# Performance work log

Measured on AMD Instinct MI355X. Metric: run time of the kernel, lower is better.

## Reference

```python
import jax, jax.numpy as jnp
import numpy as np

# ---- static geometry derived from truncation (matches torch __init__) ----
T = 127
N_LAT_NH = T + 1                                   # 128 NH latitudes
LONS = [20 + 4 * i for i in range(N_LAT_NH)]       # octahedral reduced grid
CUMS = np.concatenate([[0], np.cumsum(np.array(LONS + LONS[::-1]))]).astype(int)
HZW_NH = np.minimum(4 + np.arange(N_LAT_NH), T)    # cubic truncation: m_max = nlon//4 - 1, capped at T
N_LATS_PER_M = np.array([(HZW_NH >= m).sum() for m in range(T + 1)])
L_SYM_FULL = (T + 3) // 2                          # 65 rows before dropping row 0
L_ANT = (T + 2) // 2                               # 64
N_VARS = 128
BATCH, ENS = 4, 1


def _tri_masks():
    """Zero-padded triangular structure of the per-m Legendre matrices."""
    sym = np.zeros((T + 1, L_SYM_FULL, N_LAT_NH), np.float32)
    ant = np.zeros((T + 1, L_ANT, N_LAT_NH), np.float32)
    for m in range(T + 1):
        n_lats = int(N_LATS_PER_M[m])
        ms = (T - m + 3) // 2
        off = L_SYM_FULL - ms
        sym[m, off:, N_LAT_NH - n_lats:] = 1.0
        if (m + 1) % 2 == 1:
            sym[m, off, :] = 0.0
        ma = (T - m + 2) // 2
        off = L_ANT - ma
        ant[m, off:, N_LAT_NH - n_lats:] = 1.0
        if m % 2 == 1:
            ant[m, off, :] = 0.0
    return sym[:, 1:, :], ant   # module drops first symmetric row -> [128,64,128]


def setup_inputs() -> dict:
    key = jax.random.key(0)
    k1, k2, k3 = jax.random.split(key, 3)
    n_grid = int(CUMS[-1])
    x = jax.random.normal(k1, (BATCH, ENS, n_grid, N_VARS), jnp.float32)
    sm, am = _tri_masks()
    # random stand-ins for (gaussian-weight-fused) Legendre polynomials, with the exact
    # triangular zero structure the module builds from ecTrans assets
    symmetric = jax.random.normal(k2, sm.shape, jnp.float32) * jnp.asarray(sm)
    antisymmetric = jax.random.normal(k3, am.shape, jnp.float32) * jnp.asarray(am)
    return {"x": x, "symmetric": symmetric, "antisymmetric": antisymmetric}


def reference(x, symmetric, antisymmetric):
    """Octahedral SHT forward: ragged longitudinal rfft -> hemispheric fold -> per-m Legendre matmuls.

    Returns spectrum [b, e, l, m, vars, 2] (real/imag stacked on last axis).
    """
    n_lat = 2 * N_LAT_NH
    north, south = [], []
    # loop is over structurally distinct (ragged) latitude ring lengths; NH lat i and its
    # SH mirror (lat n_lat-1-i) share nlon/truncation, so batch them in one FFT call.
    for i in range(N_LAT_NH):
        j = n_lat - 1 - i
        nlon = LONS[i]
        xn = x[:, :, CUMS[i]:CUMS[i + 1], :]           # [b,e,nlon,v]
        xs = x[:, :, CUMS[j]:CUMS[j + 1], :]
        xp = jnp.stack([xn, xs], axis=2)               # [b,e,2,nlon,v]
        f = jnp.fft.rfft(xp, axis=3) / nlon            # torch norm='forward'
        m_hi = int(HZW_NH[i]) + 1                      # keep m <= highest zonal wavenumber
        f = f[:, :, :, :m_hi, :]
        f = jnp.pad(f, ((0, 0), (0, 0), (0, 0), (0, T + 1 - m_hi), (0, 0)))
        north.append(f[:, :, 0])
        south.append(f[:, :, 1])                       # index i <-> lat n_lat-1-i: already pole-mirrored
    north = jnp.stack(north, axis=2)                   # [b,e,n_lat_nh,m,v] complex64
    south = jnp.stack(south, axis=2)
    # hemispheric symmetry of Legendre polynomials
    sym = north + south
    anti = north - south
    # per-m truncated Legendre contractions over NH latitudes (n)
    out_s = jnp.einsum('mln,benmv->belmv', symmetric, sym)     # [b,e,64,m,v]
    out_a = jnp.einsum('mln,benmv->belmv', antisymmetric, anti)
    # interleave symmetric (l-m even) and antisymmetric (l-m odd) rows -> full l axis (128)
    spec = jnp.stack([out_s, out_a], axis=3)
    b, e, L, _, M, V = spec.shape
    spec = spec.reshape(b, e, 2 * L, M, V)             # [b,e,l,m,v] complex, lower triangle zeros
    return jnp.stack([spec.real, spec.imag], axis=-1)  # real view [b,e,l,m,v,2]
```

## Files before the change

### kernel.cpp

```cpp
#include <hip/hip_runtime.h>
#include <hip/hip_bf16.h>

#define NGRID 70144
#define NV 128

typedef float f32x4 __attribute__((ext_vector_type(4)));
typedef short short8 __attribute__((ext_vector_type(8)));

__device__ __forceinline__ float4 f4add(float4 a, float4 b){ return make_float4(a.x+b.x, a.y+b.y, a.z+b.z, a.w+b.w); }
__device__ __forceinline__ float4 f4sub(float4 a, float4 b){ return make_float4(a.x-b.x, a.y-b.y, a.z-b.z, a.w-b.w); }

__device__ __forceinline__ unsigned f2bf(float f){
  return (unsigned)__bfloat16_as_ushort(__float2bfloat16(f));
}
__device__ __forceinline__ float bf2f(unsigned h){ return __uint_as_float(h<<16); }
__device__ __forceinline__ unsigned packsplit(float f){
  unsigned h = f2bf(f);
  unsigned l = f2bf(f - bf2f(h));
  return (h<<16) | l;
}
__device__ __forceinline__ int swzc(int c){ return (c ^ (c>>3)) & 7; }

__device__ __forceinline__ void unpack_frag(int4 a, int4 b, short8 &bh, short8 &bl){
  int h0 = (int)(((unsigned)a.x >> 16) | ((unsigned)a.y & 0xFFFF0000u));
  int h1 = (int)(((unsigned)a.z >> 16) | ((unsigned)a.w & 0xFFFF0000u));
  int h2 = (int)(((unsigned)b.x >> 16) | ((unsigned)b.y & 0xFFFF0000u));
  int h3 = (int)(((unsigned)b.z >> 16) | ((unsigned)b.w & 0xFFFF0000u));
  int l0 = (int)(((unsigned)a.x & 0xFFFFu) | ((unsigned)a.y << 16));
  int l1 = (int)(((unsigned)a.z & 0xFFFFu) | ((unsigned)a.w << 16));
  int l2 = (int)(((unsigned)b.x & 0xFFFFu) | ((unsigned)b.y << 16));
  int l3 = (int)(((unsigned)b.z & 0xFFFFu) | ((unsigned)b.w << 16));
  int4 H = make_int4(h0,h1,h2,h3), L = make_int4(l0,l1,l2,l3);
  bh = *(short8*)&H; bl = *(short8*)&L;
}

struct TileT { unsigned char ring, type, mc; };
constexpr int calc_ntiles(){
  int n=0;
  for(int r=0;r<128;r++){
    int mhi=(5+r<128)?(5+r):128;
    int mtn=(mhi+15)/16;
    n += 2*((mtn+3)/4);
  }
  return n;
}
constexpr int NTILES = calc_ntiles();
struct Tiles { TileT t[NTILES]; };
constexpr Tiles make_tiles(){
  Tiles T{}; int k=0;
  for(int r=127;r>=0;r--){
    int mhi=(5+r<128)?(5+r):128;
    int mtn=(mhi+15)/16;
    int nc=(mtn+3)/4;
    for(int mc=0;mc<nc;mc++)
      for(int tp=0;tp<2;tp++){
        T.t[k].ring=(unsigned char)r; T.t[k].type=(unsigned char)tp; T.t[k].mc=(unsigned char)mc; k++;
      }
  }
  return T;
}
__constant__ Tiles TILES = make_tiles();

struct Offs { long o[129]; };
constexpr Offs make_offs(){
  Offs O{}; long off=0;
  for(int r=0;r<128;r++){
    O.o[r]=off;
    int mh=(5+r<128)?(5+r):128, jc=11+2*r;
    off += 4L*(((mh+15)/16)*16)*(((jc+31)/32)*32);
  }
  O.o[128]=off;
  return O;
}
__constant__ Offs TWOFF = make_offs();
constexpr long TWATOT = make_offs().o[128];

__global__ void fill_tw(unsigned short* __restrict__ twA){
  int ring = blockIdx.x, t = blockIdx.y;
  int N = 20+4*ring, H = N/2, JC = H+1;
  int mhi = (5+ring<128)?(5+ring):128;
  int Mpad = ((mhi+15)>>4)<<4;
  int Kpad = ((JC+31)>>5)<<5;
  long MK = (long)Mpad*Kpad;
  unsigned short* hiT = twA + TWOFF.o[ring] + (long)(t*2)*MK;
  unsigned short* loT = hiT + MK;
  float invN = 1.0f/(float)N;
  int tid = threadIdx.x;
  for(int m=0;m<Mpad;m++){
    int p0   = (int)(((long)m*tid) % N);
    int step = (int)(((long)m*256) % N);
    int p = p0;
    for(int j=tid;j<Kpad;j+=256){
      float val = 0.f;
      if(m < mhi && j < JC){
        float th = 6.2831853071795864f * (float)p * invN;
        float sn, cs; __sincosf(th,&sn,&cs);
        val = (t ? -sn : cs) * invN;
      }
      unsigned h = f2bf(val);
      unsigned l = f2bf(val - bf2f(h));
      long idx = (long)m*Kpad + j;
      hiT[idx] = (unsigned short)h;
      loT[idx] = (unsigned short)l;
      p += step; if(p>=N) p-=N;
    }
  }
}

__global__ __launch_bounds__(256,3) void dft_mfma(const float* __restrict__ x,
                                                  const unsigned short* __restrict__ twA,
                                                  unsigned* __restrict__ Gp){
  TileT tl = TILES.t[blockIdx.x];
  int ring = tl.ring, type = tl.type;
  int b = blockIdx.y;
  int N = 20+4*ring, H = N/2, JC = H+1;
  int mhi = (5+ring<128)?(5+ring):128;
  int MtN = (mhi+15)>>4;
  int Mt0 = tl.mc*4;
  int KT = (JC+31)>>5;
  int Kpad = KT<<5;
  int Mpad = MtN<<4;

  long MK = (long)Mpad*Kpad;
  const unsigned short* Ahi = twA + TWOFF.o[ring] + (long)(type*2)*MK;
  const unsigned short* Alo = Ahi + MK;

  const float* xn = x + ((long)b*NGRID + (long)ring*(2*ring+18))*NV;
  long a1 = ring+1;
  const float* xs = x + ((long)b*NGRID + (NGRID - a1*(2*a1+18)))*NV;

  __shared__ __align__(16) unsigned Bp[8192];

  int tid = threadIdx.x;
  int jb = tid >> 5, vp = tid & 31;
  int wave = tid >> 6, lane = tid & 63;
  int jj = lane & 15, kb = lane >> 4;

  f32x4 acc[4][4];
  #pragma unroll
  for(int Mt=0;Mt<4;Mt++)
    #pragma unroll
    for(int ct=0;ct<4;ct++) acc[Mt][ct] = (f32x4){0.f,0.f,0.f,0.f};

  for(int kt=0; kt<KT; ++kt){
    __syncthreads();
    float4 fS[4], fA[4];
    #pragma unroll
    for(int dj=0;dj<4;dj++){
      int j = kt*32 + jb*4 + dj;
      float4 z = make_float4(0.f,0.f,0.f,0.f);
      float4 nj=z, sj=z, np=z, sp=z;
      if(j < JC){
        nj = *(const float4*)&xn[(long)j*NV + vp*4];
        sj = *(const float4*)&xs[(long)j*NV + vp*4];
        if(j > 0 && j < H){
          int jp = N - j;
          np = *(const float4*)&xn[(long)jp*NV + vp*4];
          sp = *(const float4*)&xs[(long)jp*NV + vp*4];
        }
      }
      float4 e  = f4add(nj, sj), o  = f4sub(nj, sj);
      float4 ep = f4add(np, sp), op = f4sub(np, sp);
      fS[dj] = type ? f4sub(e, ep) : f4add(e, ep);
      fA[dj] = type ? f4sub(o, op) : f4add(o, op);
    }
    #pragma unroll
    for(int dv=0;dv<4;dv++){
      int c0 = (vp*4+dv)*2;
      int4 wS = make_int4((int)packsplit(((const float*)&fS[0])[dv]),
                          (int)packsplit(((const float*)&fS[1])[dv]),
                          (int)packsplit(((const float*)&fS[2])[dv]),
                          (int)packsplit(((const float*)&fS[3])[dv]));
      *(int4*)&Bp[c0*32 + ((jb*4) ^ (swzc(c0)<<2))] = wS;
      int c1 = c0 + 1;
      int4 wA = make_int4((int)packsplit(((const float*)&fA[0])[dv]),
                          (int)packsplit(((const float*)&fA[1])[dv]),
                          (int)packsplit(((const float*)&fA[2])[dv]),
                          (int)packsplit(((const float*)&fA[3])[dv]));
      *(int4*)&Bp[c1*32 + ((jb*4) ^ (swzc(c1)<<2))] = wA;
    }
    __syncthreads();
    short8 bh[4], bl[4];
    #pragma unroll
    for(int ct=0;ct<4;ct++){
      int c = wave*64 + ct*16 + jj;
      int sw = swzc(c)<<2;
      int4 pa = *(const int4*)&Bp[c*32 + ((kb*8) ^ sw)];
      int4 pb = *(const int4*)&Bp[c*32 + ((kb*8+4) ^ sw)];
      unpack_frag(pa, pb, bh[ct], bl[ct]);
    }
    #pragma unroll
    for(int Mt=0;Mt<4;Mt++){
      if(Mt0+Mt < MtN){
        long ao = (long)((Mt0+Mt)*16 + jj)*Kpad + kt*32 + kb*8;
        short8 ah = *(const short8*)&Ahi[ao];
        short8 al = *(const short8*)&Alo[ao];
        #pragma unroll
        for(int ct=0;ct<4;ct++){
          acc[Mt][ct] = __builtin_amdgcn_mfma_f32_16x16x32_bf16(ah, bh[ct], acc[Mt][ct], 0,0,0);
          acc[Mt][ct] = __builtin_amdgcn_mfma_f32_16x16x32_bf16(al, bh[ct], acc[Mt][ct], 0,0,0);
          acc[Mt][ct] = __builtin_amdgcn_mfma_f32_16x16x32_bf16(ah, bl[ct], acc[Mt][ct], 0,0,0);
        }
      }
    }
  }
  #pragma unroll
  for(int Mt=0;Mt<4;Mt++){
    if(Mt0+Mt < MtN){
      #pragma unroll
      for(int ct=0;ct<4;ct++){
        int c = wave*64 + ct*16 + jj;
        int s = c & 1, v = c >> 1;
        #pragma unroll
        for(int reg=0;reg<4;reg++){
          int m = (Mt0+Mt)*16 + (kb<<2) + reg;
          if(m < mhi){
            Gp[(long)((s*2+type)*128 + m)*65536 + (long)ring*512 + b*128 + v]
              = packsplit(acc[Mt][ct][reg]);
          }
        }
      }
    }
  }
}

__global__ void w_split(const float* __restrict__ Wsym, const float* __restrict__ Want,
                        unsigned short* __restrict__ Wh, unsigned short* __restrict__ Wl){
  long i = (long)blockIdx.x*256 + threadIdx.x;
  const float* W = (i < 1048576) ? Wsym : Want;
  float w = W[i & 1048575];
  unsigned h = f2bf(w);
  unsigned l = f2bf(w - bf2f(h));
  Wh[i] = (unsigned short)h;
  Wl[i] = (unsigned short)l;
}

__global__ __launch_bounds__(256) void legendre_mfma(const unsigned short* __restrict__ Wh,
                                                     const unsigned short* __restrict__ Wl,
                                                     const unsigned* __restrict__ Gp,
                                                     float* __restrict__ out){
  int m = blockIdx.x, b = blockIdx.y, s = blockIdx.z;
  __shared__ __align__(16) unsigned Bp[8192];
  int tid = threadIdx.x;
  int wave = tid >> 6, lane = tid & 63;
  int jj = lane & 15, kb = lane >> 4;

  int kt0 = (m > 4) ? ((m-4) >> 5) : 0;

  const unsigned short* WA = Wh + (long)(s*128+m)*8192;
  const unsigned short* WB = Wl + (long)(s*128+m)*8192;
  int ri = tid & 1, v = tid >> 1;
  long gC0 = (long)((s*2+ri)*128 + m)*65536 + (long)b*128 + v;

  f32x4 acc[4][4];
  #pragma unroll
  for(int a=0;a<4;a++)
    #pragma unroll
    for(int q=0;q<4;q++) acc[a][q] = (f32x4){0.f,0.f,0.f,0.f};

  int swT = swzc(tid)<<2;
  for(int kt=kt0; kt<4; ++kt){
    __syncthreads();
    #pragma unroll
    for(int k4=0;k4<32;k4+=4){
      int4 w = make_int4((int)Gp[gC0 + (long)(kt*32+k4+0)*512],
                         (int)Gp[gC0 + (long)(kt*32+k4+1)*512],
                         (int)Gp[gC0 + (long)(kt*32+k4+2)*512],
                         (int)Gp[gC0 + (long)(kt*32+k4+3)*512]);
      *(int4*)&Bp[tid*32 + (k4 ^ swT)] = w;
    }
    __syncthreads();
    short8 bh[4], bl[4];
    #pragma unroll
    for(int nt=0;nt<4;nt++){
      int c = (wave*4+nt)*16 + jj;
      int sw = swzc(c)<<2;
      int4 pa = *(const int4*)&Bp[c*32 + ((kb*8) ^ sw)];
      int4 pb = *(const int4*)&Bp[c*32 + ((kb*8+4) ^ sw)];
      unpack_frag(pa, pb, bh[nt], bl[nt]);
    }
    #pragma unroll
    for(int Mt=0;Mt<4;Mt++){
      long ao = (long)(Mt*16 + jj)*128 + kt*32 + kb*8;
      short8 ah = *(const short8*)&WA[ao];
      short8 al = *(const short8*)&WB[ao];
      #pragma unroll
      for(int nt=0;nt<4;nt++){
        acc[Mt][nt] = __builtin_amdgcn_mfma_f32_16x16x32_bf16(ah, bh[nt], acc[Mt][nt], 0,0,0);
        acc[Mt][nt] = __builtin_amdgcn_mfma_f32_16x16x32_bf16(al, bh[nt], acc[Mt][nt], 0,0,0);
        acc[Mt][nt] = __builtin_amdgcn_mfma_f32_16x16x32_bf16(ah, bl[nt], acc[Mt][nt], 0,0,0);
      }
    }
  }
  int r4 = (lane>>4)<<2;
  #pragma unroll
  for(int Mt=0;Mt<4;Mt++){
    #pragma unroll
    for(int nt=0;nt<4;nt++){
      int c = (wave*4+nt)*16 + jj;
      #pragma unroll
      for(int reg=0;reg<4;reg++){
        int l = Mt*16 + r4 + reg;
        out[((long)(b*128 + 2*l + s)*128 + m)*256 + c] = acc[Mt][nt][reg];
      }
    }
  }
}

extern "C" void kernel_launch(void* const* d_in, const int* in_sizes, int n_in,
                              void* d_out, int out_size, void* d_ws, size_t ws_size,
                              hipStream_t stream) {
  const float* x    = (const float*)d_in[0];
  const float* Wsym = (const float*)d_in[1];
  const float* Want = (const float*)d_in[2];
  float* out = (float*)d_out;

  size_t gpOffB = (size_t)TWATOT*2;
  if(gpOffB < 8388608) gpOffB = 8388608;
  gpOffB = (gpOffB + 255) & ~(size_t)255;

  unsigned short* twA = (unsigned short*)d_ws;
  unsigned* Gp = (unsigned*)((char*)d_ws + gpOffB);
  unsigned short* Wh = (unsigned short*)d_ws;
  unsigned short* Wl = Wh + 2097152;

  hipLaunchKernelGGL(fill_tw,       dim3(128,2),     dim3(256), 0, stream, twA);
  hipLaunchKernelGGL(dft_mfma,      dim3(NTILES,4),  dim3(256), 0, stream, x, twA, Gp);
  hipLaunchKernelGGL(w_split,       dim3(8192),      dim3(256), 0, stream, Wsym, Want, Wh, Wl);
  hipLaunchKernelGGL(legendre_mfma, dim3(128,4,2),   dim3(256), 0, stream, Wh, Wl, Gp, out);
}
```

Baseline: 386.5 us.

## Split DFT tiles by variable half, group rings, parallelize twiddle fill

Each DFT tile now covers half of the 128 variables, which halves the accumulators and the LDS staging buffer and doubles the number of blocks. Tiles are grouped in sets of 8 rings with padding slots that exit early, interleaving variants across neighbouring rings. The twiddle-fill kernel is also split across 4 m-slices to add parallelism. The aim is higher occupancy and better load balance. The cost is that the twiddle matrix A is loaded twice and there are more global loads of float2 width.

```diff
diff --git a/kernel.cpp b/kernel.cpp
--- a/kernel.cpp
+++ b/kernel.cpp
@@ -6,9 +6,6 @@
 
 typedef float f32x4 __attribute__((ext_vector_type(4)));
 typedef short short8 __attribute__((ext_vector_type(8)));
-
-__device__ __forceinline__ float4 f4add(float4 a, float4 b){ return make_float4(a.x+b.x, a.y+b.y, a.z+b.z, a.w+b.w); }
-__device__ __forceinline__ float4 f4sub(float4 a, float4 b){ return make_float4(a.x-b.x, a.y-b.y, a.z-b.z, a.w-b.w); }
 
 __device__ __forceinline__ unsigned f2bf(float f){
   return (unsigned)__bfloat16_as_ushort(__float2bfloat16(f));
@@ -34,27 +31,41 @@
   bh = *(short8*)&H; bl = *(short8*)&L;
 }
 
-struct TileT { unsigned char ring, type, mc; };
+struct TileT { unsigned char ring, mc, type, vh; };
+constexpr int nvar_of(int r){
+  int mhi=(5+r<128)?(5+r):128;
+  int mtn=(mhi+15)/16;
+  int nch=(mtn+3)/4;
+  return nch*4;
+}
 constexpr int calc_ntiles(){
-  int n=0;
-  for(int r=0;r<128;r++){
-    int mhi=(5+r<128)?(5+r):128;
-    int mtn=(mhi+15)/16;
-    n += 2*((mtn+3)/4);
-  }
-  return n;
+  int tot=0;
+  for(int g=0; g<16; g++){
+    int mv=0;
+    for(int q=0;q<8;q++){ int nv=nvar_of(127-(g*8+q)); if(nv>mv) mv=nv; }
+    tot += 8*mv;
+  }
+  return tot;
 }
 constexpr int NTILES = calc_ntiles();
 struct Tiles { TileT t[NTILES]; };
 constexpr Tiles make_tiles(){
   Tiles T{}; int k=0;
-  for(int r=127;r>=0;r--){
-    int mhi=(5+r<128)?(5+r):128;
-    int mtn=(mhi+15)/16;
-    int nc=(mtn+3)/4;
-    for(int mc=0;mc<nc;mc++)
-      for(int tp=0;tp<2;tp++){
-        T.t[k].ring=(unsigned char)r; T.t[k].type=(unsigned char)tp; T.t[k].mc=(unsigned char)mc; k++;
+  for(int g=0; g<16; g++){
+    int mv=0;
+    for(int q=0;q<8;q++){ int nv=nvar_of(127-(g*8+q)); if(nv>mv) mv=nv; }
+    for(int var=0; var<mv; var++)
+      for(int q=0;q<8;q++){
+        int r = 127-(g*8+q);
+        if(var < nvar_of(r)){
+          T.t[k].ring=(unsigned char)r;
+          T.t[k].mc  =(unsigned char)(var>>2);
+          T.t[k].type=(unsigned char)((var>>1)&1);
+          T.t[k].vh  =(unsigned char)(var&1);
+        } else {
+          T.t[k].ring=255;
+        }
+        k++;
       }
   }
   return T;
@@ -76,7 +87,7 @@
 constexpr long TWATOT = make_offs().o[128];
 
 __global__ void fill_tw(unsigned short* __restrict__ twA){
-  int ring = blockIdx.x, t = blockIdx.y;
+  int ring = blockIdx.x, t = blockIdx.y, mq = blockIdx.z;
   int N = 20+4*ring, H = N/2, JC = H+1;
   int mhi = (5+ring<128)?(5+ring):128;
   int Mpad = ((mhi+15)>>4)<<4;
@@ -86,7 +97,7 @@
   unsigned short* loT = hiT + MK;
   float invN = 1.0f/(float)N;
   int tid = threadIdx.x;
-  for(int m=0;m<Mpad;m++){
+  for(int m=mq; m<Mpad; m+=4){
     int p0   = (int)(((long)m*tid) % N);
     int step = (int)(((long)m*256) % N);
     int p = p0;
@@ -107,11 +118,12 @@
   }
 }
 
-__global__ __launch_bounds__(256,3) void dft_mfma(const float* __restrict__ x,
-                                                  const unsigned short* __restrict__ twA,
-                                                  unsigned* __restrict__ Gp){
+__global__ __launch_bounds__(256) void dft_mfma(const float* __restrict__ x,
+                                                const unsigned short* __restrict__ twA,
+                                                unsigned* __restrict__ Gp){
   TileT tl = TILES.t[blockIdx.x];
-  int ring = tl.ring, type = tl.type;
+  if(tl.ring == 255) return;
+  int ring = tl.ring, type = tl.type, vh = tl.vh;
   int b = blockIdx.y;
   int N = 20+4*ring, H = N/2, JC = H+1;
   int mhi = (5+ring<128)?(5+ring):128;
@@ -129,61 +141,65 @@
   long a1 = ring+1;
   const float* xs = x + ((long)b*NGRID + (NGRID - a1*(2*a1+18)))*NV;
 
-  __shared__ __align__(16) unsigned Bp[8192];
+  __shared__ __align__(16) unsigned Bp[4096];
 
   int tid = threadIdx.x;
-  int jb = tid >> 5, vp = tid & 31;
+  int jb = tid >> 5;
+  int vp = tid & 31;
+  int vo = vh*64 + vp*2;
   int wave = tid >> 6, lane = tid & 63;
   int jj = lane & 15, kb = lane >> 4;
 
-  f32x4 acc[4][4];
+  f32x4 acc[4][2];
   #pragma unroll
-  for(int Mt=0;Mt<4;Mt++)
-    #pragma unroll
-    for(int ct=0;ct<4;ct++) acc[Mt][ct] = (f32x4){0.f,0.f,0.f,0.f};
+  for(int Mt=0;Mt<4;Mt++){ acc[Mt][0]=(f32x4){0.f,0.f,0.f,0.f}; acc[Mt][1]=(f32x4){0.f,0.f,0.f,0.f}; }
 
   for(int kt=0; kt<KT; ++kt){
     __syncthreads();
-    float4 fS[4], fA[4];
+    float gSx[4], gSy[4], gAx[4], gAy[4];
     #pragma unroll
     for(int dj=0;dj<4;dj++){
       int j = kt*32 + jb*4 + dj;
-      float4 z = make_float4(0.f,0.f,0.f,0.f);
-      float4 nj=z, sj=z, np=z, sp=z;
+      float2 nj=make_float2(0.f,0.f), sj=nj, np=nj, sp=nj;
       if(j < JC){
-        nj = *(const float4*)&xn[(long)j*NV + vp*4];
-        sj = *(const float4*)&xs[(long)j*NV + vp*4];
+        nj = *(const float2*)&xn[(long)j*NV + vo];
+        sj = *(const float2*)&xs[(long)j*NV + vo];
         if(j > 0 && j < H){
           int jp = N - j;
-          np = *(const float4*)&xn[(long)jp*NV + vp*4];
-          sp = *(const float4*)&xs[(long)jp*NV + vp*4];
+          np = *(const float2*)&xn[(long)jp*NV + vo];
+          sp = *(const float2*)&xs[(long)jp*NV + vo];
         }
       }
-      float4 e  = f4add(nj, sj), o  = f4sub(nj, sj);
-      float4 ep = f4add(np, sp), op = f4sub(np, sp);
-      fS[dj] = type ? f4sub(e, ep) : f4add(e, ep);
-      fA[dj] = type ? f4sub(o, op) : f4add(o, op);
-    }
-    #pragma unroll
-    for(int dv=0;dv<4;dv++){
-      int c0 = (vp*4+dv)*2;
-      int4 wS = make_int4((int)packsplit(((const float*)&fS[0])[dv]),
-                          (int)packsplit(((const float*)&fS[1])[dv]),
-                          (int)packsplit(((const float*)&fS[2])[dv]),
-                          (int)packsplit(((const float*)&fS[3])[dv]));
-      *(int4*)&Bp[c0*32 + ((jb*4) ^ (swzc(c0)<<2))] = wS;
-      int c1 = c0 + 1;
-      int4 wA = make_int4((int)packsplit(((const float*)&fA[0])[dv]),
-                          (int)packsplit(((const float*)&fA[1])[dv]),
-                          (int)packsplit(((const float*)&fA[2])[dv]),
-                          (int)packsplit(((const float*)&fA[3])[dv]));
-      *(int4*)&Bp[c1*32 + ((jb*4) ^ (swzc(c1)<<2))] = wA;
+      float ex=nj.x+sj.x, ey=nj.y+sj.y, ox=nj.x-sj.x, oy=nj.y-sj.y;
+      float epx=np.x+sp.x, epy=np.y+sp.y, opx=np.x-sp.x, opy=np.y-sp.y;
+      gSx[dj] = type ? (ex-epx) : (ex+epx);
+      gSy[dj] = type ? (ey-epy) : (ey+epy);
+      gAx[dj] = type ? (ox-opx) : (ox+opx);
+      gAy[dj] = type ? (oy-opy) : (oy+opy);
+    }
+    {
+      int c0 = (vp*2)*2;
+      int4 w0 = make_int4((int)packsplit(gSx[0]),(int)packsplit(gSx[1]),
+                          (int)packsplit(gSx[2]),(int)packsplit(gSx[3]));
+      *(int4*)&Bp[c0*32 + ((jb*4) ^ (swzc(c0)<<2))] = w0;
+      int c1 = c0+1;
+      int4 w1 = make_int4((int)packsplit(gAx[0]),(int)packsplit(gAx[1]),
+                          (int)packsplit(gAx[2]),(int)packsplit(gAx[3]));
+      *(int4*)&Bp[c1*32 + ((jb*4) ^ (swzc(c1)<<2))] = w1;
+      int c2 = c0+2;
+      int4 w2 = make_int4((int)packsplit(gSy[0]),(int)packsplit(gSy[1]),
+                          (int)packsplit(gSy[2]),(int)packsplit(gSy[3]));
+      *(int4*)&Bp[c2*32 + ((jb*4) ^ (swzc(c2)<<2))] = w2;
+      int c3 = c0+3;
+      int4 w3 = make_int4((int)packsplit(gAy[0]),(int)packsplit(gAy[1]),
+                          (int)packsplit(gAy[2]),(int)packsplit(gAy[3]));
+      *(int4*)&Bp[c3*32 + ((jb*4) ^ (swzc(c3)<<2))] = w3;
     }
     __syncthreads();
-    short8 bh[4], bl[4];
-    #pragma unroll
-    for(int ct=0;ct<4;ct++){
-      int c = wave*64 + ct*16 + jj;
+    short8 bh[2], bl[2];
+    #pragma unroll
+    for(int ct=0;ct<2;ct++){
+      int c = wave*32 + ct*16 + jj;
       int sw = swzc(c)<<2;
       int4 pa = *(const int4*)&Bp[c*32 + ((kb*8) ^ sw)];
       int4 pb = *(const int4*)&Bp[c*32 + ((kb*8+4) ^ sw)];
@@ -196,7 +212,7 @@
         short8 ah = *(const short8*)&Ahi[ao];
         short8 al = *(const short8*)&Alo[ao];
         #pragma unroll
-        for(int ct=0;ct<4;ct++){
+        for(int ct=0;ct<2;ct++){
           acc[Mt][ct] = __builtin_amdgcn_mfma_f32_16x16x32_bf16(ah, bh[ct], acc[Mt][ct], 0,0,0);
           acc[Mt][ct] = __builtin_amdgcn_mfma_f32_16x16x32_bf16(al, bh[ct], acc[Mt][ct], 0,0,0);
           acc[Mt][ct] = __builtin_amdgcn_mfma_f32_16x16x32_bf16(ah, bl[ct], acc[Mt][ct], 0,0,0);
@@ -208,9 +224,9 @@
   for(int Mt=0;Mt<4;Mt++){
     if(Mt0+Mt < MtN){
       #pragma unroll
-      for(int ct=0;ct<4;ct++){
-        int c = wave*64 + ct*16 + jj;
-        int s = c & 1, v = c >> 1;
+      for(int ct=0;ct<2;ct++){
+        int cg = vh*128 + wave*32 + ct*16 + jj;
+        int s = cg & 1, v = cg >> 1;
         #pragma unroll
         for(int reg=0;reg<4;reg++){
           int m = (Mt0+Mt)*16 + (kb<<2) + reg;
@@ -324,7 +340,7 @@
   unsigned short* Wh = (unsigned short*)d_ws;
   unsigned short* Wl = Wh + 2097152;
 
-  hipLaunchKernelGGL(fill_tw,       dim3(128,2),     dim3(256), 0, stream, twA);
+  hipLaunchKernelGGL(fill_tw,       dim3(128,2,4),   dim3(256), 0, stream, twA);
   hipLaunchKernelGGL(dft_mfma,      dim3(NTILES,4),  dim3(256), 0, stream, x, twA, Gp);
   hipLaunchKernelGGL(w_split,       dim3(8192),      dim3(256), 0, stream, Wsym, Want, Wh, Wl);
   hipLaunchKernelGGL(legendre_mfma, dim3(128,4,2),   dim3(256), 0, stream, Wh, Wl, Gp, out);
```

Result: faster. 358.8 us (-7.2%).
